# Kernel tuning notes

Measured on AMD Instinct MI355X. Metric: run time of the kernel, lower is better.

The kernel has to match this reference:

```python
import jax, jax.numpy as jnp
import numpy as np
import math

N_TOK = 8192; IN_DIM = 1024; D = 512; HEADS = 8; DH = D // HEADS
M = D // 2; ITERS = 6; SCALE = DH ** -0.5; KRES = 33; NCLS = 2
EPS = 1e-5


def ln(x, g, b):
    mu = jnp.mean(x, -1, keepdims=True)
    var = jnp.var(x, -1, keepdims=True)
    return (x - mu) * jax.lax.rsqrt(var + EPS) * g + b


def moore_penrose_pinv(x):
    # Newton-Schulz iterative pseudo-inverse (lucidrains nystrom-attention)
    col = jnp.abs(x).sum(-1).max()
    row = jnp.abs(x).sum(-2).max()
    z = jnp.swapaxes(x, -1, -2) / (col * row)
    I = jnp.eye(x.shape[-1], dtype=x.dtype)
    for _ in range(ITERS):
        xz = x @ z
        z = 0.25 * z @ (13 * I - xz @ (15 * I - xz @ (7 * I - xz)))
    return z


def nystrom_attn(x, qkv_w, out_w, out_b, conv_w):
    b, n, _ = x.shape
    pad = (-n) % M  # pad at FRONT so seq len divisible by num_landmarks
    xp = jnp.pad(x, ((0, 0), (pad, 0), (0, 0)))
    Np = n + pad
    q, k, v = jnp.split(xp @ qkv_w, 3, axis=-1)
    tohead = lambda t: t.reshape(b, Np, HEADS, DH).transpose(0, 2, 1, 3)  # bhnd
    q = tohead(q) * SCALE; k = tohead(k); v = tohead(v)
    l = Np // M
    q_l = q.reshape(b, HEADS, M, l, DH).mean(3)  # landmark means, bhmd
    k_l = k.reshape(b, HEADS, M, l, DH).mean(3)
    a1 = jax.nn.softmax(jnp.einsum('bhnd,bhmd->bhnm', q, k_l), -1)
    a2 = jax.nn.softmax(jnp.einsum('bhnd,bhmd->bhnm', q_l, k_l), -1)
    a3 = jax.nn.softmax(jnp.einsum('bhmd,bhnd->bhmn', q_l, k), -1)
    out = (a1 @ moore_penrose_pinv(a2)) @ (a3 @ v)
    pc = KRES // 2  # depthwise residual conv over sequence dim (groups=heads)
    out = out + jax.lax.conv_general_dilated(
        v, conv_w, (1, 1), [(pc, pc), (0, 0)],
        dimension_numbers=('NCHW', 'OIHW', 'NCHW'), feature_group_count=HEADS)
    out = out.transpose(0, 2, 1, 3).reshape(b, Np, D)
    return (out @ out_w + out_b)[:, -n:]


def ppeg(x, Hs, Ws, w7, b7, w5, b5, w3, b3):
    b, _, C = x.shape
    cls_tok, feat = x[:, :1], x[:, 1:]
    f = feat.transpose(0, 2, 1).reshape(b, C, Hs, Ws)
    def dw(w, bb, p):
        return jax.lax.conv_general_dilated(
            f, w, (1, 1), [(p, p), (p, p)],
            dimension_numbers=('NCHW', 'OIHW', 'NCHW'),
            feature_group_count=C) + bb[None, :, None, None]
    y = f + dw(w7, b7, 3) + dw(w5, b5, 2) + dw(w3, b3, 1)
    y = y.reshape(b, C, Hs * Ws).transpose(0, 2, 1)
    return jnp.concatenate([cls_tok, y], axis=1)


def setup_inputs() -> dict:
    key = jax.random.key(0)
    ks = jax.random.split(key, 16)
    s = 0.02
    return {
        'x': jax.random.normal(ks[0], (N_TOK, IN_DIM), jnp.float32),
        'fc1_w': jax.random.normal(ks[1], (IN_DIM, D), jnp.float32) * s,
        'fc1_b': jnp.zeros((D,), jnp.float32),
        'cls_token': jax.random.normal(ks[2], (1, 1, D), jnp.float32),
        'ln1_g': jnp.ones((D,), jnp.float32), 'ln1_b': jnp.zeros((D,), jnp.float32),
        'qkv1_w': jax.random.normal(ks[3], (D, 3 * D), jnp.float32) * s,
        'out1_w': jax.random.normal(ks[4], (D, D), jnp.float32) * s,
        'out1_b': jnp.zeros((D,), jnp.float32),
        'conv1_w': jax.random.normal(ks[5], (HEADS, 1, KRES, 1), jnp.float32) * s,
        'ln2_g': jnp.ones((D,), jnp.float32), 'ln2_b': jnp.zeros((D,), jnp.float32),
        'qkv2_w': jax.random.normal(ks[6], (D, 3 * D), jnp.float32) * s,
        'out2_w': jax.random.normal(ks[7], (D, D), jnp.float32) * s,
        'out2_b': jnp.zeros((D,), jnp.float32),
        'conv2_w': jax.random.normal(ks[8], (HEADS, 1, KRES, 1), jnp.float32) * s,
        'pg7_w': jax.random.normal(ks[9], (D, 1, 7, 7), jnp.float32) * s,
        'pg7_b': jnp.zeros((D,), jnp.float32),
        'pg5_w': jax.random.normal(ks[10], (D, 1, 5, 5), jnp.float32) * s,
        'pg5_b': jnp.zeros((D,), jnp.float32),
        'pg3_w': jax.random.normal(ks[11], (D, 1, 3, 3), jnp.float32) * s,
        'pg3_b': jnp.zeros((D,), jnp.float32),
        'norm_g': jnp.ones((D,), jnp.float32), 'norm_b': jnp.zeros((D,), jnp.float32),
        'fc2_w': jax.random.normal(ks[12], (D, NCLS), jnp.float32) * s,
        'fc2_b': jnp.zeros((NCLS,), jnp.float32),
    }


def reference(x, fc1_w, fc1_b, cls_token, ln1_g, ln1_b, qkv1_w, out1_w, out1_b,
              conv1_w, ln2_g, ln2_b, qkv2_w, out2_w, out2_b, conv2_w,
              pg7_w, pg7_b, pg5_w, pg5_b, pg3_w, pg3_b, norm_g, norm_b,
              fc2_w, fc2_b):
    h = jax.nn.relu(x[None].astype(jnp.float32) @ fc1_w + fc1_b)  # [1,N,D]
    n = h.shape[1]
    Hs = Ws = int(math.ceil(math.sqrt(n)))
    add = Hs * Ws - n
    h = jnp.concatenate([h, h[:, :add]], axis=1)  # pad to square by duplication
    h = jnp.concatenate([jnp.broadcast_to(cls_token, (1, 1, D)), h], axis=1)
    h = h + nystrom_attn(ln(h, ln1_g, ln1_b), qkv1_w, out1_w, out1_b, conv1_w)
    h = ppeg(h, Hs, Ws, pg7_w, pg7_b, pg5_w, pg5_b, pg3_w, pg3_b)
    h = h + nystrom_attn(ln(h, ln2_g, ln2_b), qkv2_w, out2_w, out2_b, conv2_w)
    emb = ln(h, norm_g, norm_b)[:, 0]  # cls embedding [1,D]
    logits = emb @ fc2_w + fc2_b
    Y_prob = jax.nn.softmax(logits, -1)
    Y_hat = jnp.argmax(logits, -1)
    return (logits, Y_prob, Y_hat, emb)
```

## Files before the change

### kernel.cpp

```cpp
#include <hip/hip_runtime.h>
#include <math.h>

#define NTOK   8192
#define INDIM  1024
#define NHEAD  8
#define N1     8282
#define NP     8448
#define PAD    166
#define LCH    33
#define SCALE  0.125f
#define HS     91
#define KSPLIT 24
#define KCH    (NP / KSPLIT)

typedef __attribute__((ext_vector_type(8))) _Float16 half8;
typedef __attribute__((ext_vector_type(8))) short short8;
typedef __attribute__((ext_vector_type(4))) float f32x4;
typedef unsigned short ushort_t;

#define GPTR(p) ((const __attribute__((address_space(1))) void*)(p))
#define LPTR(p) ((__attribute__((address_space(3))) void*)(p))

__device__ __forceinline__ ushort_t f2h(float f) {
    union { _Float16 h; ushort_t u; } v; v.h = (_Float16)f;
    return v.u;
}
__device__ __forceinline__ float h2f(ushort_t u) {
    union { ushort_t u; _Float16 h; } v; v.u = u;
    return (float)v.h;
}


__device__ __forceinline__ float blockReduceSumF(float v, float* red, int tid) {
    red[tid] = v; __syncthreads();
    for (int s = 128; s > 0; s >>= 1) {
        if (tid < s) red[tid] += red[tid + s];
        __syncthreads();
    }
    float r = red[0]; __syncthreads();
    return r;
}
__device__ __forceinline__ float blockReduceMaxF(float v, float* red, int tid) {
    red[tid] = v; __syncthreads();
    for (int s = 128; s > 0; s >>= 1) {
        if (tid < s) red[tid] = fmaxf(red[tid], red[tid + s]);
        __syncthreads();
    }
    float r = red[0]; __syncthreads();
    return r;
}

__global__ void zero_k(float* __restrict__ p)
{
    int i = blockIdx.x * 256 + threadIdx.x;
    reinterpret_cast<float4*>(p)[i] = make_float4(0.f, 0.f, 0.f, 0.f);
}

__global__ __launch_bounds__(256) void tcast_k(const float* __restrict__ w, ushort_t* __restrict__ wT,
                                               int K, int N)
{
    __shared__ float tb[32][33];
    int tx = threadIdx.x & 31, ty = threadIdx.x >> 5;
    int n0 = blockIdx.x * 32, k0 = blockIdx.y * 32;
#pragma unroll
    for (int i = 0; i < 4; ++i)
        tb[ty + i * 8][tx] = w[(size_t)(k0 + ty + i * 8) * N + n0 + tx];
    __syncthreads();
#pragma unroll
    for (int i = 0; i < 4; ++i)
        wT[(size_t)(n0 + ty + i * 8) * K + k0 + tx] = f2h(tb[tx][ty + i * 8]);
}

__global__ void bcast_k(const float* __restrict__ x, ushort_t* __restrict__ o)
{
    int i = blockIdx.x * 256 + threadIdx.x;
    float4 v = reinterpret_cast<const float4*>(x)[i];
    ushort4 u;
    u.x = f2h(v.x); u.y = f2h(v.y); u.z = f2h(v.z); u.w = f2h(v.w);
    reinterpret_cast<ushort4*>(o)[i] = u;
}

__global__ __launch_bounds__(256) void gemm_mn_f16(
    const ushort_t* __restrict__ A, const ushort_t* __restrict__ BT,
    const float* __restrict__ bias, const float* __restrict__ res,
    float* __restrict__ C, ushort_t* __restrict__ Ch,
    int Mvalid, int K, int lda, int ldb, int ldc, int relu, int qscale)
{
    __shared__ ushort_t As[128 * 32];
    __shared__ ushort_t Bs[64 * 32];
    const int tid = threadIdx.x;
    const int wave = tid >> 6, lane = tid & 63;
    const int row0 = blockIdx.y * 128, col0 = blockIdx.x * 64;
    const int wr = wave * 32;
    const int aRow = wave * 16 + (lane >> 2);
    const int aChS = (((lane & 3) ^ ((lane >> 3) & 3)) * 8);
    const int bRow = tid >> 2;
    const int bChS = (((tid & 3) ^ ((tid >> 3) & 3)) * 8);
    const int lr = lane & 15, lq = (lane >> 4) * 4;
    const int lks = (((lane >> 4) ^ ((lr >> 1) & 3)) * 8);
    f32x4 acc[2][4] = {};
    for (int k0 = 0; k0 < K; k0 += 32) {
        __syncthreads();
#pragma unroll
        for (int i = 0; i < 2; ++i) {
            const ushort_t* gp = A + (size_t)(row0 + i * 64 + aRow) * lda + k0 + aChS;
            __builtin_amdgcn_global_load_lds(GPTR(gp), LPTR(As + (i * 64 + wave * 16) * 32), 16, 0, 0);
        }
        const ushort_t* gq = BT + (size_t)(col0 + bRow) * ldb + k0 + bChS;
        __builtin_amdgcn_global_load_lds(GPTR(gq), LPTR(Bs + tid * 8), 16, 0, 0);
        __syncthreads();
        half8 af[2], bfr[4];
#pragma unroll
        for (int mi = 0; mi < 2; ++mi)
            af[mi] = *reinterpret_cast<const half8*>(&As[(wr + mi * 16 + lr) * 32 + lks]);
#pragma unroll
        for (int ni = 0; ni < 4; ++ni)
            bfr[ni] = *reinterpret_cast<const half8*>(&Bs[(ni * 16 + lr) * 32 + lks]);
#pragma unroll
        for (int mi = 0; mi < 2; ++mi)
#pragma unroll
            for (int ni = 0; ni < 4; ++ni)
                acc[mi][ni] = __builtin_amdgcn_mfma_f32_16x16x32_f16(af[mi], bfr[ni], acc[mi][ni], 0, 0, 0);
    }
#pragma unroll
    for (int mi = 0; mi < 2; ++mi) {
#pragma unroll
        for (int q = 0; q < 4; ++q) {
            int r = row0 + wr + mi * 16 + lq + q;
            if (r >= Mvalid) continue;
#pragma unroll
            for (int ni = 0; ni < 4; ++ni) {
                int c = col0 + ni * 16 + lr;
                float v = acc[mi][ni][q];
                if (bias) v += bias[c];
                if (res)  v += res[(size_t)r * ldc + c];
                if (relu) v = fmaxf(v, 0.f);
                if (Ch) {
                    if (qscale && c < 512) v *= SCALE;
                    Ch[(size_t)r * ldc + c] = f2h(v);
                } else {
                    C[(size_t)r * ldc + c] = v;
                }
            }
        }
    }
}

__global__ __launch_bounds__(256) void bgemm64_f16(
    const ushort_t* __restrict__ A, const ushort_t* __restrict__ B,
    ushort_t* __restrict__ C, float diag, float ss,
    ushort_t* __restrict__ C2, float diag2, float ss2)
{
    __shared__ ushort_t As[64 * 32];
    __shared__ ushort_t Bs[64 * 32];
    const int h = blockIdx.z;
    const ushort_t* Ah = A + (size_t)h * 65536;
    const ushort_t* Bh = B + (size_t)h * 65536;
    const int tid = threadIdx.x;
    const int wave = tid >> 6, lane = tid & 63;
    const int row0 = blockIdx.y * 64, col0 = blockIdx.x * 64;
    const int wr = (wave >> 1) * 32, wc = (wave & 1) * 32;
    const int aRow = tid >> 2;
    const int aChS = (((tid & 3) ^ ((tid >> 3) & 3)) * 8);
    const int kp = (tid >> 3) & 15, nc = tid & 7;
    const int kk = (kp * 2) ^ ((nc & 3) << 3);
    const int lr = lane & 15, lk = (lane >> 4) * 8, lq = (lane >> 4) * 4;
    const int lks = (((lane >> 4) ^ ((lr >> 1) & 3)) * 8);
    f32x4 acc[2][2] = {};
    for (int k0 = 0; k0 < 256; k0 += 32) {
        __syncthreads();
        const ushort_t* gp = Ah + (size_t)(row0 + aRow) * 256 + k0 + aChS;
        __builtin_amdgcn_global_load_lds(GPTR(gp), LPTR(As + tid * 8), 16, 0, 0);
        if (tid < 128) {
            const ushort_t* bp = Bh + (size_t)(k0 + kp * 2) * 256 + col0 + nc * 8;
            short8 v0 = *reinterpret_cast<const short8*>(bp);
            short8 v1 = *reinterpret_cast<const short8*>(bp + 256);
#pragma unroll
            for (int j = 0; j < 8; ++j) {
                unsigned int pk = ((unsigned int)(ushort_t)v1[j] << 16) | (unsigned int)(ushort_t)v0[j];
                *reinterpret_cast<unsigned int*>(&Bs[(nc * 8 + j) * 32 + kk]) = pk;
            }
        }
        __syncthreads();
        half8 af[2], bfr[2];
#pragma unroll
        for (int mi = 0; mi < 2; ++mi)
            af[mi] = *reinterpret_cast<const half8*>(&As[(wr + mi * 16 + lr) * 32 + lks]);
#pragma unroll
        for (int ni = 0; ni < 2; ++ni) {
            int nn = wc + ni * 16 + lr;
            bfr[ni] = *reinterpret_cast<const half8*>(&Bs[nn * 32 + (lk ^ (((nn >> 3) & 3) << 3))]);
        }
#pragma unroll
        for (int mi = 0; mi < 2; ++mi)
#pragma unroll
            for (int ni = 0; ni < 2; ++ni)
                acc[mi][ni] = __builtin_amdgcn_mfma_f32_16x16x32_f16(af[mi], bfr[ni], acc[mi][ni], 0, 0, 0);
    }
    ushort_t* Chp = C + (size_t)h * 65536;
#pragma unroll
    for (int mi = 0; mi < 2; ++mi)
#pragma unroll
        for (int ni = 0; ni < 2; ++ni)
#pragma unroll
            for (int q = 0; q < 4; ++q) {
                int r = row0 + wr + mi * 16 + lq + q;
                int c = col0 + wc + ni * 16 + lr;
                float v = ss * acc[mi][ni][q];
                if (r == c) v += diag;
                Chp[(size_t)r * 256 + c] = f2h(v);
                if (C2) {
                    float v2 = ss2 * acc[mi][ni][q];
                    if (r == c) v2 += diag2;
                    C2[(size_t)h * 65536 + (size_t)r * 256 + c] = f2h(v2);
                }
            }
}

__global__ __launch_bounds__(256) void hgemm_abT_k(
    const ushort_t* __restrict__ A, long sAh, int lda,
    const ushort_t* __restrict__ BT, long sBh, int ldb,
    ushort_t* __restrict__ C, long sCh, int ldc, int K,
    float* __restrict__ rsum, int sRsum)
{
    __shared__ ushort_t As[128 * 32];
    __shared__ ushort_t Bs[128 * 32];
    const int h = blockIdx.z;
    const ushort_t* Ah = A + (size_t)h * sAh;
    const ushort_t* Bh = BT + (size_t)h * sBh;
    ushort_t* Chp = C + (size_t)h * sCh;
    const int tid = threadIdx.x;
    const int wave = tid >> 6, lane = tid & 63;
    const int row0 = blockIdx.y * 128, col0 = blockIdx.x * 128;
    const int wr = (wave >> 1) * 64, wc = (wave & 1) * 64;
    const int sRow = wave * 16 + (lane >> 2);
    const int sChS = (((lane & 3) ^ ((lane >> 3) & 3)) * 8);
    const int lr = lane & 15, lq = (lane >> 4) * 4;
    const int lks = (((lane >> 4) ^ ((lr >> 1) & 3)) * 8);
    f32x4 acc[4][4] = {};
    for (int k0 = 0; k0 < K; k0 += 32) {
        __syncthreads();
#pragma unroll
        for (int i = 0; i < 2; ++i) {
            const ushort_t* gp = Ah + (size_t)(row0 + i * 64 + sRow) * lda + k0 + sChS;
            __builtin_amdgcn_global_load_lds(GPTR(gp), LPTR(As + (i * 64 + wave * 16) * 32), 16, 0, 0);
            const ushort_t* gq = Bh + (size_t)(col0 + i * 64 + sRow) * ldb + k0 + sChS;
            __builtin_amdgcn_global_load_lds(GPTR(gq), LPTR(Bs + (i * 64 + wave * 16) * 32), 16, 0, 0);
        }
        __syncthreads();
        half8 af[4], bfr[4];
#pragma unroll
        for (int mi = 0; mi < 4; ++mi)
            af[mi] = *reinterpret_cast<const half8*>(&As[(wr + mi * 16 + lr) * 32 + lks]);
#pragma unroll
        for (int ni = 0; ni < 4; ++ni)
            bfr[ni] = *reinterpret_cast<const half8*>(&Bs[(wc + ni * 16 + lr) * 32 + lks]);
#pragma unroll
        for (int mi = 0; mi < 4; ++mi)
#pragma unroll
            for (int ni = 0; ni < 4; ++ni)
                acc[mi][ni] = __builtin_amdgcn_mfma_f32_16x16x32_f16(af[mi], bfr[ni], acc[mi][ni], 0, 0, 0);
    }
#pragma unroll
    for (int mi = 0; mi < 4; ++mi)
#pragma unroll
        for (int q = 0; q < 4; ++q) {
            int r = row0 + wr + mi * 16 + lq + q;
            float s = 0.f;
#pragma unroll
            for (int ni = 0; ni < 4; ++ni) {
                float e = __expf(acc[mi][ni][q]);
                Chp[(size_t)r * ldc + col0 + wc + ni * 16 + lr] = f2h(e);
                s += e;
            }
            for (int off = 8; off; off >>= 1) s += __shfl_xor(s, off, 64);
            if (lr == 0) atomicAdd(&rsum[(size_t)h * sRsum + r], s);
        }
}

__global__ __launch_bounds__(256) void fa1_k(
    const ushort_t* __restrict__ qkv16, const ushort_t* __restrict__ kl,
    const ushort_t* __restrict__ W, ushort_t* __restrict__ attn)
{
    __shared__ ushort_t Pl[128][264];
    __shared__ ushort_t As[128 * 32];
    __shared__ ushort_t Bs[64 * 32];
    __shared__ float rs_l[128];
    const int h = blockIdx.y;
    const int row0 = blockIdx.x * 128;
    const ushort_t* Aq = qkv16 + h * 64;
    const ushort_t* klh = kl + (size_t)h * 16384;
    const ushort_t* Wh = W + (size_t)h * 16384;
    const int tid = threadIdx.x;
    const int wave = tid >> 6, lane = tid & 63;
    const int wr = wave * 32;
    const int aRow = wave * 16 + (lane >> 2);
    const int aChS = (((lane & 3) ^ ((lane >> 3) & 3)) * 8);
    const int bRow = tid >> 2;
    const int bChS = (((tid & 3) ^ ((tid >> 3) & 3)) * 8);
    const int lr = lane & 15, lk = (lane >> 4) * 8, lq = (lane >> 4) * 4;
    const int lks = (((lane >> 4) ^ ((lr >> 1) & 3)) * 8);
    const int kp = (tid >> 3) & 15, ncs = tid & 7;
    const int kk = (kp * 2) ^ ((ncs & 3) << 3);
    float rs[2][4] = {};
    for (int nc0 = 0; nc0 < 256; nc0 += 64) {
        f32x4 acc[2][4] = {};
        for (int k0 = 0; k0 < 64; k0 += 32) {
            __syncthreads();
#pragma unroll
            for (int i = 0; i < 2; ++i) {
                const ushort_t* gp = Aq + (size_t)(row0 + i * 64 + aRow) * 1536 + k0 + aChS;
                __builtin_amdgcn_global_load_lds(GPTR(gp), LPTR(As + (i * 64 + wave * 16) * 32), 16, 0, 0);
            }
            const ushort_t* gq = klh + (size_t)(nc0 + bRow) * 64 + k0 + bChS;
            __builtin_amdgcn_global_load_lds(GPTR(gq), LPTR(Bs + tid * 8), 16, 0, 0);
            __syncthreads();
            half8 af[2], bfr[4];
#pragma unroll
            for (int mi = 0; mi < 2; ++mi)
                af[mi] = *reinterpret_cast<const half8*>(&As[(wr + mi * 16 + lr) * 32 + lks]);
#pragma unroll
            for (int ni = 0; ni < 4; ++ni)
                bfr[ni] = *reinterpret_cast<const half8*>(&Bs[(ni * 16 + lr) * 32 + lks]);
#pragma unroll
            for (int mi = 0; mi < 2; ++mi)
#pragma unroll
                for (int ni = 0; ni < 4; ++ni)
                    acc[mi][ni] = __builtin_amdgcn_mfma_f32_16x16x32_f16(af[mi], bfr[ni], acc[mi][ni], 0, 0, 0);
        }
#pragma unroll
        for (int mi = 0; mi < 2; ++mi)
#pragma unroll
            for (int q = 0; q < 4; ++q) {
                int r = wr + mi * 16 + lq + q;
                float s = 0.f;
#pragma unroll
                for (int ni = 0; ni < 4; ++ni) {
                    float e = __expf(acc[mi][ni][q]);
                    Pl[r][nc0 + ni * 16 + lr] = f2h(e);
                    s += e;
                }
                for (int off = 8; off; off >>= 1) s += __shfl_xor(s, off, 64);
                rs[mi][q] += s;
            }
    }
    if (lr == 0) {
#pragma unroll
        for (int mi = 0; mi < 2; ++mi)
#pragma unroll
            for (int q = 0; q < 4; ++q)
                rs_l[wr + mi * 16 + lq + q] = rs[mi][q];
    }
    __syncthreads();
    f32x4 acc[2][4] = {};
    for (int k0 = 0; k0 < 256; k0 += 32) {
        __syncthreads();
        if (tid < 128) {
            const ushort_t* bp = Wh + (size_t)(k0 + kp * 2) * 64 + ncs * 8;
            short8 v0 = *reinterpret_cast<const short8*>(bp);
            short8 v1 = *reinterpret_cast<const short8*>(bp + 64);
#pragma unroll
            for (int j = 0; j < 8; ++j) {
                unsigned int pk = ((unsigned int)(ushort_t)v1[j] << 16) | (unsigned int)(ushort_t)v0[j];
                *reinterpret_cast<unsigned int*>(&Bs[(ncs * 8 + j) * 32 + kk]) = pk;
            }
        }
        __syncthreads();
        half8 af[2], bfr[4];
#pragma unroll
        for (int mi = 0; mi < 2; ++mi)
            af[mi] = *reinterpret_cast<const half8*>(&Pl[wr + mi * 16 + lr][k0 + lk]);
#pragma unroll
        for (int ni = 0; ni < 4; ++ni) {
            int nn = ni * 16 + lr;
            bfr[ni] = *reinterpret_cast<const half8*>(&Bs[nn * 32 + (lk ^ (((nn >> 3) & 3) << 3))]);
        }
#pragma unroll
        for (int mi = 0; mi < 2; ++mi)
#pragma unroll
            for (int ni = 0; ni < 4; ++ni)
                acc[mi][ni] = __builtin_amdgcn_mfma_f32_16x16x32_f16(af[mi], bfr[ni], acc[mi][ni], 0, 0, 0);
    }
#pragma unroll
    for (int mi = 0; mi < 2; ++mi)
#pragma unroll
        for (int q = 0; q < 4; ++q) {
            int rloc = wr + mi * 16 + lq + q;
            int t = row0 + rloc;
            float inv = 1.f / rs_l[rloc];
#pragma unroll
            for (int ni = 0; ni < 4; ++ni)
                attn[(size_t)t * 512 + h * 64 + ni * 16 + lr] = f2h(acc[mi][ni][q] * inv);
        }
}

__global__ __launch_bounds__(256) void hgemm_pv_k(
    const ushort_t* __restrict__ P, const ushort_t* __restrict__ qkv16,
    float* __restrict__ part)
{
    __shared__ ushort_t As[128 * 32];
    __shared__ ushort_t Bs[64 * 32];
    const int ks = blockIdx.x, row0 = blockIdx.y * 128, h = blockIdx.z;
    const ushort_t* Ph = P + (size_t)h * 256 * NP;
    const ushort_t* V = qkv16 + 1024 + h * 64;
    const int tid = threadIdx.x;
    const int wave = tid >> 6, lane = tid & 63;
    const int wr = wave * 32;
    const int sRow = wave * 16 + (lane >> 2);
    const int sChS = (((lane & 3) ^ ((lane >> 3) & 3)) * 8);
    const int lr = lane & 15, lk = (lane >> 4) * 8, lq = (lane >> 4) * 4;
    const int lks = (((lane >> 4) ^ ((lr >> 1) & 3)) * 8);
    const int kp = (tid >> 3) & 15, nc = tid & 7;
    const int kk = (kp * 2) ^ ((nc & 3) << 3);
    f32x4 acc[2][4] = {};
    for (int k0 = ks * KCH; k0 < (ks + 1) * KCH; k0 += 32) {
        __syncthreads();
#pragma unroll
        for (int i = 0; i < 2; ++i) {
            const ushort_t* gp = Ph + (size_t)(row0 + i * 64 + sRow) * NP + k0 + sChS;
            __builtin_amdgcn_global_load_lds(GPTR(gp), LPTR(As + (i * 64 + wave * 16) * 32), 16, 0, 0);
        }
        if (tid < 128) {
            const ushort_t* bp = V + (size_t)(k0 + kp * 2) * 1536 + nc * 8;
            short8 v0 = *reinterpret_cast<const short8*>(bp);
            short8 v1 = *reinterpret_cast<const short8*>(bp + 1536);
#pragma unroll
            for (int j = 0; j < 8; ++j) {
                unsigned int pk = ((unsigned int)(ushort_t)v1[j] << 16) | (unsigned int)(ushort_t)v0[j];
                *reinterpret_cast<unsigned int*>(&Bs[(nc * 8 + j) * 32 + kk]) = pk;
            }
        }
        __syncthreads();
        half8 af[2], bfr[4];
#pragma unroll
        for (int mi = 0; mi < 2; ++mi)
            af[mi] = *reinterpret_cast<const half8*>(&As[(wr + mi * 16 + lr) * 32 + lks]);
#pragma unroll
        for (int ni = 0; ni < 4; ++ni) {
            int nn = ni * 16 + lr;
            bfr[ni] = *reinterpret_cast<const half8*>(&Bs[nn * 32 + (lk ^ (((nn >> 3) & 3) << 3))]);
        }
#pragma unroll
        for (int mi = 0; mi < 2; ++mi)
#pragma unroll
            for (int ni = 0; ni < 4; ++ni)
                acc[mi][ni] = __builtin_amdgcn_mfma_f32_16x16x32_f16(af[mi], bfr[ni], acc[mi][ni], 0, 0, 0);
    }
    float* pp = part + ((size_t)(ks * 8 + h) * 256) * 64;
#pragma unroll
    for (int mi = 0; mi < 2; ++mi)
#pragma unroll
        for (int q = 0; q < 4; ++q) {
            int r = row0 + wr + mi * 16 + lq + q;
#pragma unroll
            for (int ni = 0; ni < 4; ++ni)
                pp[(size_t)r * 64 + ni * 16 + lr] = acc[mi][ni][q];
        }
}

__global__ __launch_bounds__(256) void pv_reduce_k(const float* __restrict__ part,
                                                   const float* __restrict__ rsum,
                                                   ushort_t* __restrict__ av)
{
    int idx = blockIdx.x * 256 + threadIdx.x;
    int rc = idx >> 6;
    float s = 0.f;
#pragma unroll
    for (int ks = 0; ks < KSPLIT; ++ks)
        s += part[(size_t)ks * 131072 + idx];
    av[idx] = f2h(s / rsum[rc]);
}

__global__ __launch_bounds__(256) void wmat_k(const ushort_t* __restrict__ z,
                                              const ushort_t* __restrict__ av,
                                              ushort_t* __restrict__ W)
{
    int idx = blockIdx.x * 4 + (threadIdx.x >> 6);
    int h = idx >> 8, m = idx & 255, d = threadIdx.x & 63;
    const ushort_t* zp = z + (size_t)h * 65536 + (size_t)m * 256;
    const ushort_t* ap = av + (size_t)h * 16384 + d;
    float acc = 0.f;
    for (int j = 0; j < 256; ++j) acc += h2f(zp[j]) * h2f(ap[(size_t)j * 64]);
    W[((size_t)h * 256 + m) * 64 + d] = f2h(acc);
}

__global__ void fixup_k(const float* __restrict__ cls, float* __restrict__ h)
{
    int i = blockIdx.x * 256 + threadIdx.x;
    if (i < 512) {
        h[i] = cls[i];
    } else {
        int j = i - 512;
        h[(size_t)8193 * 512 + j] = h[512 + j];
    }
}

__global__ __launch_bounds__(256) void ln_pad_k(
    const float* __restrict__ h, const float* __restrict__ g, const float* __restrict__ b,
    ushort_t* __restrict__ out)
{
    int row = blockIdx.x, tid = threadIdx.x;
    __shared__ float red[256];
    ushort_t* o = out + (size_t)row * 512;
    if (row < PAD) { o[tid] = 0; o[tid + 256] = 0; return; }
    const float* x = h + (size_t)(row - PAD) * 512;
    float v0 = x[tid], v1 = x[tid + 256];
    float mu = blockReduceSumF(v0 + v1, red, tid) * (1.f / 512.f);
    float d0 = v0 - mu, d1 = v1 - mu;
    float var = blockReduceSumF(d0 * d0 + d1 * d1, red, tid) * (1.f / 512.f);
    float rstd = rsqrtf(var + 1e-5f);
    o[tid]       = f2h(d0 * rstd * g[tid] + b[tid]);
    o[tid + 256] = f2h(d1 * rstd * g[tid + 256] + b[tid + 256]);
}

__global__ __launch_bounds__(256) void landmark_k(const ushort_t* __restrict__ qkv,
                                                  ushort_t* __restrict__ ql,
                                                  ushort_t* __restrict__ kl)
{
    int idx = blockIdx.x * 4 + (threadIdx.x >> 6);
    int h = idx >> 8, m = idx & 255, d = threadIdx.x & 63;
    const ushort_t* base = qkv + (size_t)(m * LCH) * 1536 + h * 64 + d;
    float sq = 0.f, sk = 0.f;
    for (int i = 0; i < LCH; ++i) {
        sq += h2f(base[(size_t)i * 1536]);
        sk += h2f(base[(size_t)i * 1536 + 512]);
    }
    ql[((size_t)h * 256 + m) * 64 + d] = f2h(sq * (1.f / (float)LCH));
    kl[((size_t)h * 256 + m) * 64 + d] = f2h(sk * (1.f / (float)LCH));
}

__global__ __launch_bounds__(256) void a2_k(
    const ushort_t* __restrict__ ql, const ushort_t* __restrict__ kl, ushort_t* __restrict__ a2)
{
    int h = blockIdx.x >> 8, r = blockIdx.x & 255, tid = threadIdx.x;
    __shared__ float qv[64]; __shared__ float red[256];
    if (tid < 64) qv[tid] = h2f(ql[((size_t)h * 256 + r) * 64 + tid]);
    __syncthreads();
    const ushort_t* kp = kl + ((size_t)h * 256 + tid) * 64;
    float dot = 0.f;
#pragma unroll
    for (int d = 0; d < 64; ++d) dot += qv[d] * h2f(kp[d]);
    float mx = blockReduceMaxF(dot, red, tid);
    float e = expf(dot - mx);
    float s = blockReduceSumF(e, red, tid);
    a2[((size_t)h * 256 + r) * 256 + tid] = f2h(e / s);
}

__global__ __launch_bounds__(256) void colsum_k(const ushort_t* __restrict__ a2, float* __restrict__ cs)
{
    int h = blockIdx.x >> 8, c = blockIdx.x & 255;
    __shared__ float red[256];
    float v = fabsf(h2f(a2[(size_t)h * 65536 + (size_t)threadIdx.x * 256 + c]));
    float s = blockReduceSumF(v, red, threadIdx.x);
    if (!threadIdx.x) cs[blockIdx.x] = s;
}
__global__ __launch_bounds__(256) void pinv_scal_k(const float* __restrict__ cs, float* __restrict__ scal)
{
    int tid = threadIdx.x; __shared__ float red[256];
    float m2 = -1e30f;
    for (int i = tid; i < 2048; i += 256) m2 = fmaxf(m2, cs[i]);
    m2 = blockReduceMaxF(m2, red, tid);
    if (!tid) scal[0] = 1.f / m2;
}
__global__ __launch_bounds__(256) void zinit_k(const ushort_t* __restrict__ a2, const float* __restrict__ scal,
                                               ushort_t* __restrict__ z)
{
    int h = blockIdx.x >> 8, r = blockIdx.x & 255, c = threadIdx.x;
    z[(size_t)h * 65536 + (size_t)r * 256 + c] =
        f2h(h2f(a2[(size_t)h * 65536 + (size_t)c * 256 + r]) * scal[0]);
}

#define CTT 64
__global__ __launch_bounds__(256) void conv2_k(const ushort_t* __restrict__ qkv,
                                               const float* __restrict__ cw,
                                               ushort_t* __restrict__ attn)
{
    __shared__ float vt[CTT + 32][64];
    int t0 = blockIdx.x * CTT;
    int h = blockIdx.y;
    int tid = threadIdx.x;
    for (int s = tid; s < (CTT + 32) * 8; s += 256) {
        int row = s >> 3, q8 = s & 7;
        int tt = t0 - 16 + row;
        if (tt >= 0 && tt < NP) {
            short8 v = *reinterpret_cast<const short8*>(qkv + (size_t)tt * 1536 + 1024 + h * 64 + q8 * 8);
#pragma unroll
            for (int j = 0; j < 8; ++j) vt[row][q8 * 8 + j] = h2f((ushort_t)v[j]);
        } else {
#pragma unroll
            for (int j = 0; j < 8; ++j) vt[row][q8 * 8 + j] = 0.f;
        }
    }
    float w33[33];
#pragma unroll
    for (int j = 0; j < 33; ++j) w33[j] = cw[h * 33 + j];
    __syncthreads();
    int c = tid & 63, tr = tid >> 6;
    float win[48];
#pragma unroll
    for (int j = 0; j < 48; ++j) win[j] = vt[tr * 16 + j][c];
#pragma unroll
    for (int i = 0; i < 16; ++i) {
        float acc = 0.f;
#pragma unroll
        for (int j = 0; j < 33; ++j) acc += w33[j] * win[i + j];
        size_t idx = (size_t)(t0 + tr * 16 + i) * 512 + h * 64 + c;
        attn[idx] = f2h(h2f(attn[idx]) + acc);
    }
}

#define PTS  16
#define PIT  22
#define PITT (PIT*PIT)
#define PCG  8
#define PSTR 12
__global__ __launch_bounds__(256) void ppeg_tiled_k(
    const float* __restrict__ hin,
    const float* __restrict__ w7, const float* __restrict__ b7,
    const float* __restrict__ w5, const float* __restrict__ b5,
    const float* __restrict__ w3, const float* __restrict__ b3,
    float* __restrict__ hout)
{
    __shared__ float inb[PITT][PSTR];
    __shared__ float wcT[49][PCG];
    __shared__ float bs[PCG];
    int tid = threadIdx.x;
    int c0 = blockIdx.z * PCG;
    int ty0 = blockIdx.y * PTS, tx0 = blockIdx.x * PTS;
    if (blockIdx.x == 0 && blockIdx.y == 0 && tid < PCG)
        hout[c0 + tid] = hin[c0 + tid];
    for (int idx = tid; idx < PITT * 2; idx += 256) {
        int tok = idx >> 1, q = idx & 1;
        int gy = ty0 - 3 + tok / PIT, gx = tx0 - 3 + tok % PIT;
        float4 v = make_float4(0.f, 0.f, 0.f, 0.f);
        if (gy >= 0 && gy < HS && gx >= 0 && gx < HS)
            v = *reinterpret_cast<const float4*>(hin + (size_t)(1 + gy * HS + gx) * 512 + c0 + q * 4);
        *reinterpret_cast<float4*>(&inb[tok][q * 4]) = v;
    }
    for (int idx = tid; idx < PCG * 49; idx += 256) {
        int c = idx / 49, t = idx % 49;
        int ky = t / 7, kx = t % 7, dy = ky - 3, dx = kx - 3;
        float w = w7[(size_t)(c0 + c) * 49 + t];
        if (dy >= -2 && dy <= 2 && dx >= -2 && dx <= 2)
            w += w5[(size_t)(c0 + c) * 25 + (dy + 2) * 5 + (dx + 2)];
        if (dy >= -1 && dy <= 1 && dx >= -1 && dx <= 1)
            w += w3[(size_t)(c0 + c) * 9 + (dy + 1) * 3 + (dx + 1)];
        wcT[t][c] = w;
    }
    if (tid < PCG) bs[tid] = b7[c0 + tid] + b5[c0 + tid] + b3[c0 + tid];
    __syncthreads();
    int oy = tid >> 4, ox = tid & 15;
    int gy = ty0 + oy, gx = tx0 + ox;
    if (gy >= HS || gx >= HS) return;
    float acc[PCG];
    {
        const float* cp = &inb[(oy + 3) * PIT + ox + 3][0];
        float4 i0 = *reinterpret_cast<const float4*>(cp);
        float4 i1 = *reinterpret_cast<const float4*>(cp + 4);
        acc[0] = i0.x + bs[0]; acc[1] = i0.y + bs[1]; acc[2] = i0.z + bs[2]; acc[3] = i0.w + bs[3];
        acc[4] = i1.x + bs[4]; acc[5] = i1.y + bs[5]; acc[6] = i1.z + bs[6]; acc[7] = i1.w + bs[7];
    }
#pragma unroll
    for (int ky = 0; ky < 7; ++ky)
#pragma unroll
        for (int kx = 0; kx < 7; ++kx) {
            int t = ky * 7 + kx;
            const float* dp = &inb[(oy + ky) * PIT + ox + kx][0];
            float4 d0 = *reinterpret_cast<const float4*>(dp);
            float4 d1 = *reinterpret_cast<const float4*>(dp + 4);
            float4 w0 = *reinterpret_cast<const float4*>(&wcT[t][0]);
            float4 w1 = *reinterpret_cast<const float4*>(&wcT[t][4]);
            acc[0] += w0.x * d0.x; acc[1] += w0.y * d0.y;
            acc[2] += w0.z * d0.z; acc[3] += w0.w * d0.w;
            acc[4] += w1.x * d1.x; acc[5] += w1.y * d1.y;
            acc[6] += w1.z * d1.z; acc[7] += w1.w * d1.w;
        }
    float* out = hout + (size_t)(1 + gy * HS + gx) * 512 + c0;
    *reinterpret_cast<float4*>(out)     = make_float4(acc[0], acc[1], acc[2], acc[3]);
    *reinterpret_cast<float4*>(out + 4) = make_float4(acc[4], acc[5], acc[6], acc[7]);
}

__global__ __launch_bounds__(256) void final_k(const float* __restrict__ h,
                                               const float* __restrict__ g, const float* __restrict__ bb,
                                               const float* __restrict__ w, const float* __restrict__ fb,
                                               float* __restrict__ out)
{
    __shared__ float red[256];
    int tid = threadIdx.x;
    float v0 = h[tid], v1 = h[tid + 256];
    float mu = blockReduceSumF(v0 + v1, red, tid) * (1.f / 512.f);
    float d0 = v0 - mu, d1 = v1 - mu;
    float var = blockReduceSumF(d0 * d0 + d1 * d1, red, tid) * (1.f / 512.f);
    float rstd = rsqrtf(var + 1e-5f);
    float e0 = d0 * rstd * g[tid] + bb[tid];
    float e1 = d1 * rstd * g[tid + 256] + bb[tid + 256];
    out[5 + tid] = e0;
    out[5 + 256 + tid] = e1;
    float l0p = e0 * w[tid * 2] + e1 * w[(tid + 256) * 2];
    float l1p = e0 * w[tid * 2 + 1] + e1 * w[(tid + 256) * 2 + 1];
    float l0 = blockReduceSumF(l0p, red, tid);
    float l1 = blockReduceSumF(l1p, red, tid);
    if (!tid) {
        l0 += fb[0]; l1 += fb[1];
        out[0] = l0; out[1] = l1;
        float mx = fmaxf(l0, l1);
        float p0 = expf(l0 - mx), p1 = expf(l1 - mx);
        float si = 1.f / (p0 + p1);
        out[2] = p0 * si; out[3] = p1 * si;
        out[4] = (l1 > l0) ? 1.f : 0.f;
    }
}

struct WsPtrs {
    float *h, *h2, *cs, *scal, *rsum3, *part;
    ushort_t *xbB, *qkv16, *ql16, *kl16, *a2h, *zh, *z2h, *xzh, *t1h, *t2h;
    ushort_t *av16, *W16, *qkvT, *outT, *x16, *fc1T, *S16;
};

static void run_attn(float* hbuf, const float* ln_g, const float* ln_b,
                     const float* qkv_w, const float* out_w, const float* out_b,
                     const float* conv_w, const WsPtrs& P, hipStream_t s)
{
    tcast_k<<<dim3(1536 / 32, 512 / 32), 256, 0, s>>>(qkv_w, P.qkvT, 512, 1536);
    tcast_k<<<dim3(512 / 32, 512 / 32), 256, 0, s>>>(out_w, P.outT, 512, 512);
    ln_pad_k<<<NP, 256, 0, s>>>(hbuf, ln_g, ln_b, P.xbB);
    gemm_mn_f16<<<dim3(1536 / 64, NP / 128), 256, 0, s>>>(P.xbB, P.qkvT, nullptr, nullptr,
                                                          nullptr, P.qkv16, NP, 512, 512, 512, 1536, 0, 1);
    landmark_k<<<512, 256, 0, s>>>(P.qkv16, P.ql16, P.kl16);
    a2_k<<<2048, 256, 0, s>>>(P.ql16, P.kl16, P.a2h);
    colsum_k<<<2048, 256, 0, s>>>(P.a2h, P.cs);
    pinv_scal_k<<<1, 256, 0, s>>>(P.cs, P.scal);
    zinit_k<<<2048, 256, 0, s>>>(P.a2h, P.scal, P.zh);
    ushort_t* za = P.zh; ushort_t* zb = P.z2h;
    for (int it = 0; it < 6; ++it) {
        bgemm64_f16<<<dim3(4, 4, 8), 256, 0, s>>>(P.a2h, za, P.xzh, 0.f, 1.f, P.t1h, 7.f, -1.f);
        bgemm64_f16<<<dim3(4, 4, 8), 256, 0, s>>>(P.xzh, P.t1h, P.t2h, 15.f, -1.f, nullptr, 0.f, 0.f);
        bgemm64_f16<<<dim3(4, 4, 8), 256, 0, s>>>(P.xzh, P.t2h, P.t1h, 13.f, -1.f, nullptr, 0.f, 0.f);
        bgemm64_f16<<<dim3(4, 4, 8), 256, 0, s>>>(za, P.t1h, zb, 0.f, 0.25f, nullptr, 0.f, 0.f);
        ushort_t* tmp = za; za = zb; zb = tmp;
    }
    zero_k<<<2, 256, 0, s>>>(P.rsum3);
    hgemm_abT_k<<<dim3(NP / 128, 2, 8), 256, 0, s>>>(P.ql16, 16384, 64,
                                                     P.qkv16 + 512, 64, 1536,
                                                     P.S16, (long)256 * NP, NP, 64,
                                                     P.rsum3, 256);
    hgemm_pv_k<<<dim3(KSPLIT, 2, 8), 256, 0, s>>>(P.S16, P.qkv16, P.part);
    pv_reduce_k<<<512, 256, 0, s>>>(P.part, P.rsum3, P.av16);
    wmat_k<<<512, 256, 0, s>>>(za, P.av16, P.W16);
    fa1_k<<<dim3(NP / 128, 8), 256, 0, s>>>(P.qkv16, P.kl16, P.W16, P.xbB);
    conv2_k<<<dim3(NP / CTT, 8), 256, 0, s>>>(P.qkv16, conv_w, P.xbB);
    gemm_mn_f16<<<dim3(512 / 64, (N1 + 127) / 128), 256, 0, s>>>(P.xbB + (size_t)PAD * 512, P.outT,
                                                                 out_b, hbuf, hbuf, nullptr,
                                                                 N1, 512, 512, 512, 512, 0, 0);
}

extern "C" void kernel_launch(void* const* d_in, const int* in_sizes, int n_in,
                              void* d_out, int out_size, void* d_ws, size_t ws_size,
                              hipStream_t stream)
{
    (void)in_sizes; (void)n_in; (void)out_size; (void)ws_size;
    const float* x       = (const float*)d_in[0];
    const float* fc1_w   = (const float*)d_in[1];
    const float* fc1_b   = (const float*)d_in[2];
    const float* cls_tok = (const float*)d_in[3];
    const float* ln1_g   = (const float*)d_in[4];
    const float* ln1_b   = (const float*)d_in[5];
    const float* qkv1_w  = (const float*)d_in[6];
    const float* out1_w  = (const float*)d_in[7];
    const float* out1_b  = (const float*)d_in[8];
    const float* conv1_w = (const float*)d_in[9];
    const float* ln2_g   = (const float*)d_in[10];
    const float* ln2_b   = (const float*)d_in[11];
    const float* qkv2_w  = (const float*)d_in[12];
    const float* out2_w  = (const float*)d_in[13];
    const float* out2_b  = (const float*)d_in[14];
    const float* conv2_w = (const float*)d_in[15];
    const float* pg7_w   = (const float*)d_in[16];
    const float* pg7_b   = (const float*)d_in[17];
    const float* pg5_w   = (const float*)d_in[18];
    const float* pg5_b   = (const float*)d_in[19];
    const float* pg3_w   = (const float*)d_in[20];
    const float* pg3_b   = (const float*)d_in[21];
    const float* norm_g  = (const float*)d_in[22];
    const float* norm_b  = (const float*)d_in[23];
    const float* fc2_w   = (const float*)d_in[24];
    const float* fc2_b   = (const float*)d_in[25];

    float* ws = (float*)d_ws;
    WsPtrs P;
    float* cur = ws;
    P.h     = cur; cur += (size_t)N1 * 512;
    P.h2    = cur; cur += (size_t)N1 * 512;
    P.xbB   = (ushort_t*)cur; cur += (size_t)NP * 512 / 2;
    P.qkv16 = (ushort_t*)cur; cur += (size_t)NP * 1536 / 2;
    P.ql16  = (ushort_t*)cur; cur += 65536;
    P.kl16  = (ushort_t*)cur; cur += 65536;
    P.a2h   = (ushort_t*)cur; cur += 262144;
    P.zh    = (ushort_t*)cur; cur += 262144;
    P.z2h   = (ushort_t*)cur; cur += 262144;
    P.xzh   = (ushort_t*)cur; cur += 262144;
    P.t1h   = (ushort_t*)cur; cur += 262144;
    P.t2h   = (ushort_t*)cur; cur += 262144;
    P.av16  = (ushort_t*)cur; cur += 65536;
    P.W16   = (ushort_t*)cur; cur += 65536;
    P.cs    = cur; cur += 2048;
    P.scal  = cur; cur += 64;
    P.qkvT  = (ushort_t*)cur; cur += 393216 + 64;
    P.outT  = (ushort_t*)cur; cur += 131072 + 64;
    P.rsum3 = cur; cur += 2048;
    P.part  = cur; cur += (size_t)KSPLIT * 131072;
    P.S16   = (ushort_t*)cur; cur += (size_t)8 * 256 * NP / 2;
    P.x16   = P.S16;
    P.fc1T  = P.S16 + (size_t)NTOK * INDIM;

    bcast_k<<<(NTOK * INDIM) / 1024, 256, 0, stream>>>(x, P.x16);
    tcast_k<<<dim3(512 / 32, 1024 / 32), 256, 0, stream>>>(fc1_w, P.fc1T, 1024, 512);
    gemm_mn_f16<<<dim3(512 / 64, NTOK / 128), 256, 0, stream>>>(P.x16, P.fc1T, fc1_b, nullptr,
                                                                P.h + 512, nullptr,
                                                                NTOK, 1024, 1024, 1024, 512, 1, 0);
    fixup_k<<<180, 256, 0, stream>>>(cls_tok, P.h);
    run_attn(P.h, ln1_g, ln1_b, qkv1_w, out1_w, out1_b, conv1_w, P, stream);
    ppeg_tiled_k<<<dim3(6, 6, 512 / PCG), 256, 0, stream>>>(P.h, pg7_w, pg7_b, pg5_w, pg5_b,
                                                            pg3_w, pg3_b, P.h2);
    run_attn(P.h2, ln2_g, ln2_b, qkv2_w, out2_w, out2_b, conv2_w, P, stream);
    final_k<<<1, 256, 0, stream>>>(P.h2, norm_g, norm_b, fc2_w, fc2_b, (float*)d_out);
}
```

Baseline: 782.4 us.

## Fuse landmark-query scores, exp and PV product into one split-K flash kernel

Replaces the separate kernel that computed exp(q_l·k^T) into a large fp16 score buffer, followed by a split-K P·V GEMM, with one kernel. Each block streams 64-token chunks of K, computes the exponentiated scores into LDS, accumulates row sums in registers and immediately multiplies by V. This avoids writing and re-reading the 8×256×8448 score matrix through global memory. In exchange the work is split 33 ways along the tokens, so partial sums grow, and each chunk now carries extra barriers.

```diff
diff --git a/kernel.cpp b/kernel.cpp
--- a/kernel.cpp
+++ b/kernel.cpp
@@ -10,8 +10,8 @@
 #define LCH    33
 #define SCALE  0.125f
 #define HS     91
-#define KSPLIT 24
-#define KCH    (NP / KSPLIT)
+#define KS3    33
+#define KC3    (NP / KS3)
 
 typedef __attribute__((ext_vector_type(8))) _Float16 half8;
 typedef __attribute__((ext_vector_type(8))) short short8;
@@ -217,65 +217,128 @@
             }
 }
 
-__global__ __launch_bounds__(256) void hgemm_abT_k(
-    const ushort_t* __restrict__ A, long sAh, int lda,
-    const ushort_t* __restrict__ BT, long sBh, int ldb,
-    ushort_t* __restrict__ C, long sCh, int ldc, int K,
-    float* __restrict__ rsum, int sRsum)
-{
-    __shared__ ushort_t As[128 * 32];
-    __shared__ ushort_t Bs[128 * 32];
-    const int h = blockIdx.z;
-    const ushort_t* Ah = A + (size_t)h * sAh;
-    const ushort_t* Bh = BT + (size_t)h * sBh;
-    ushort_t* Chp = C + (size_t)h * sCh;
+__global__ __launch_bounds__(256) void fs3_k(
+    const ushort_t* __restrict__ ql, const ushort_t* __restrict__ qkv16,
+    float* __restrict__ part, float* __restrict__ rsum)
+{
+    __shared__ ushort_t Qs[2][128 * 32];
+    __shared__ ushort_t Bs[64 * 32];
+    __shared__ ushort_t Pl[128][72];
+    const int ks = blockIdx.x, row0 = blockIdx.y * 128, h = blockIdx.z;
+    const ushort_t* Ah = ql + (size_t)h * 16384;
+    const ushort_t* Kh = qkv16 + 512 + h * 64;
+    const ushort_t* Vh = qkv16 + 1024 + h * 64;
     const int tid = threadIdx.x;
     const int wave = tid >> 6, lane = tid & 63;
-    const int row0 = blockIdx.y * 128, col0 = blockIdx.x * 128;
-    const int wr = (wave >> 1) * 64, wc = (wave & 1) * 64;
-    const int sRow = wave * 16 + (lane >> 2);
-    const int sChS = (((lane & 3) ^ ((lane >> 3) & 3)) * 8);
-    const int lr = lane & 15, lq = (lane >> 4) * 4;
+    const int wr = wave * 32;
+    const int aRow = wave * 16 + (lane >> 2);
+    const int aChS = (((lane & 3) ^ ((lane >> 3) & 3)) * 8);
+    const int bRow = tid >> 2;
+    const int bChS = (((tid & 3) ^ ((tid >> 3) & 3)) * 8);
+    const int lr = lane & 15, lk = (lane >> 4) * 8, lq = (lane >> 4) * 4;
     const int lks = (((lane >> 4) ^ ((lr >> 1) & 3)) * 8);
-    f32x4 acc[4][4] = {};
-    for (int k0 = 0; k0 < K; k0 += 32) {
-        __syncthreads();
+    const int kp = (tid >> 3) & 15, nc = tid & 7;
+    const int kk = (kp * 2) ^ ((nc & 3) << 3);
+#pragma unroll
+    for (int hh = 0; hh < 2; ++hh)
 #pragma unroll
         for (int i = 0; i < 2; ++i) {
-            const ushort_t* gp = Ah + (size_t)(row0 + i * 64 + sRow) * lda + k0 + sChS;
-            __builtin_amdgcn_global_load_lds(GPTR(gp), LPTR(As + (i * 64 + wave * 16) * 32), 16, 0, 0);
-            const ushort_t* gq = Bh + (size_t)(col0 + i * 64 + sRow) * ldb + k0 + sChS;
-            __builtin_amdgcn_global_load_lds(GPTR(gq), LPTR(Bs + (i * 64 + wave * 16) * 32), 16, 0, 0);
-        }
-        __syncthreads();
-        half8 af[4], bfr[4];
-#pragma unroll
-        for (int mi = 0; mi < 4; ++mi)
-            af[mi] = *reinterpret_cast<const half8*>(&As[(wr + mi * 16 + lr) * 32 + lks]);
-#pragma unroll
-        for (int ni = 0; ni < 4; ++ni)
-            bfr[ni] = *reinterpret_cast<const half8*>(&Bs[(wc + ni * 16 + lr) * 32 + lks]);
-#pragma unroll
-        for (int mi = 0; mi < 4; ++mi)
+            const ushort_t* gp = Ah + (size_t)(row0 + i * 64 + aRow) * 64 + hh * 32 + aChS;
+            __builtin_amdgcn_global_load_lds(GPTR(gp), LPTR(Qs[hh] + (i * 64 + wave * 16) * 32), 16, 0, 0);
+        }
+    f32x4 aco[2][4] = {};
+    float rs[2][4] = {};
+    for (int c = 0; c < KC3; c += 64) {
+        const int tok0 = ks * KC3 + c;
+        f32x4 acs[2][4] = {};
+#pragma unroll
+        for (int k0 = 0; k0 < 64; k0 += 32) {
+            __syncthreads();
+            const ushort_t* gq = Kh + (size_t)(tok0 + bRow) * 1536 + k0 + bChS;
+            __builtin_amdgcn_global_load_lds(GPTR(gq), LPTR(Bs + tid * 8), 16, 0, 0);
+            __syncthreads();
+            half8 af[2], bfr[4];
+#pragma unroll
+            for (int mi = 0; mi < 2; ++mi)
+                af[mi] = *reinterpret_cast<const half8*>(&Qs[k0 >> 5][(wr + mi * 16 + lr) * 32 + lks]);
 #pragma unroll
             for (int ni = 0; ni < 4; ++ni)
-                acc[mi][ni] = __builtin_amdgcn_mfma_f32_16x16x32_f16(af[mi], bfr[ni], acc[mi][ni], 0, 0, 0);
-    }
-#pragma unroll
-    for (int mi = 0; mi < 4; ++mi)
+                bfr[ni] = *reinterpret_cast<const half8*>(&Bs[(ni * 16 + lr) * 32 + lks]);
+#pragma unroll
+            for (int mi = 0; mi < 2; ++mi)
+#pragma unroll
+                for (int ni = 0; ni < 4; ++ni)
+                    acs[mi][ni] = __builtin_amdgcn_mfma_f32_16x16x32_f16(af[mi], bfr[ni], acs[mi][ni], 0, 0, 0);
+        }
+#pragma unroll
+        for (int mi = 0; mi < 2; ++mi)
+#pragma unroll
+            for (int q = 0; q < 4; ++q) {
+                int r = wr + mi * 16 + lq + q;
+                float s = 0.f;
+#pragma unroll
+                for (int ni = 0; ni < 4; ++ni) {
+                    float e = __expf(acs[mi][ni][q]);
+                    Pl[r][ni * 16 + lr] = f2h(e);
+                    s += e;
+                }
+                for (int off = 8; off; off >>= 1) s += __shfl_xor(s, off, 64);
+                rs[mi][q] += s;
+            }
+#pragma unroll
+        for (int k0 = 0; k0 < 64; k0 += 32) {
+            __syncthreads();
+            if (tid < 128) {
+                const ushort_t* bp = Vh + (size_t)(tok0 + k0 + kp * 2) * 1536 + nc * 8;
+                short8 v0 = *reinterpret_cast<const short8*>(bp);
+                short8 v1 = *reinterpret_cast<const short8*>(bp + 1536);
+#pragma unroll
+                for (int j = 0; j < 8; ++j) {
+                    unsigned int pk = ((unsigned int)(ushort_t)v1[j] << 16) | (unsigned int)(ushort_t)v0[j];
+                    *reinterpret_cast<unsigned int*>(&Bs[(nc * 8 + j) * 32 + kk]) = pk;
+                }
+            }
+            __syncthreads();
+            half8 af[2], bfr[4];
+#pragma unroll
+            for (int mi = 0; mi < 2; ++mi)
+                af[mi] = *reinterpret_cast<const half8*>(&Pl[wr + mi * 16 + lr][k0 + lk]);
+#pragma unroll
+            for (int ni = 0; ni < 4; ++ni) {
+                int nn = ni * 16 + lr;
+                bfr[ni] = *reinterpret_cast<const half8*>(&Bs[nn * 32 + (lk ^ (((nn >> 3) & 3) << 3))]);
+            }
+#pragma unroll
+            for (int mi = 0; mi < 2; ++mi)
+#pragma unroll
+                for (int ni = 0; ni < 4; ++ni)
+                    aco[mi][ni] = __builtin_amdgcn_mfma_f32_16x16x32_f16(af[mi], bfr[ni], aco[mi][ni], 0, 0, 0);
+        }
+    }
+    float* pp = part + (size_t)(ks * 8 + h) * 16384;
+#pragma unroll
+    for (int mi = 0; mi < 2; ++mi)
 #pragma unroll
         for (int q = 0; q < 4; ++q) {
             int r = row0 + wr + mi * 16 + lq + q;
-            float s = 0.f;
-#pragma unroll
-            for (int ni = 0; ni < 4; ++ni) {
-                float e = __expf(acc[mi][ni][q]);
-                Chp[(size_t)r * ldc + col0 + wc + ni * 16 + lr] = f2h(e);
-                s += e;
-            }
-            for (int off = 8; off; off >>= 1) s += __shfl_xor(s, off, 64);
-            if (lr == 0) atomicAdd(&rsum[(size_t)h * sRsum + r], s);
-        }
+#pragma unroll
+            for (int ni = 0; ni < 4; ++ni)
+                pp[(size_t)r * 64 + ni * 16 + lr] = aco[mi][ni][q];
+            if (lr == 0) atomicAdd(&rsum[h * 256 + r], rs[mi][q]);
+        }
+}
+
+__global__ __launch_bounds__(256) void pv_reduce_k(const float* __restrict__ part,
+                                                   const float* __restrict__ rsum,
+                                                   ushort_t* __restrict__ av)
+{
+    int idx = blockIdx.x * 256 + threadIdx.x;
+    int rc = idx >> 6;
+    float s = 0.f;
+#pragma unroll
+    for (int ks = 0; ks < KS3; ++ks)
+        s += part[(size_t)ks * 131072 + idx];
+    av[idx] = f2h(s / rsum[rc]);
 }
 
 __global__ __launch_bounds__(256) void fa1_k(
@@ -394,83 +457,6 @@
         }
 }
 
-__global__ __launch_bounds__(256) void hgemm_pv_k(
-    const ushort_t* __restrict__ P, const ushort_t* __restrict__ qkv16,
-    float* __restrict__ part)
-{
-    __shared__ ushort_t As[128 * 32];
-    __shared__ ushort_t Bs[64 * 32];
-    const int ks = blockIdx.x, row0 = blockIdx.y * 128, h = blockIdx.z;
-    const ushort_t* Ph = P + (size_t)h * 256 * NP;
-    const ushort_t* V = qkv16 + 1024 + h * 64;
-    const int tid = threadIdx.x;
-    const int wave = tid >> 6, lane = tid & 63;
-    const int wr = wave * 32;
-    const int sRow = wave * 16 + (lane >> 2);
-    const int sChS = (((lane & 3) ^ ((lane >> 3) & 3)) * 8);
-    const int lr = lane & 15, lk = (lane >> 4) * 8, lq = (lane >> 4) * 4;
-    const int lks = (((lane >> 4) ^ ((lr >> 1) & 3)) * 8);
-    const int kp = (tid >> 3) & 15, nc = tid & 7;
-    const int kk = (kp * 2) ^ ((nc & 3) << 3);
-    f32x4 acc[2][4] = {};
-    for (int k0 = ks * KCH; k0 < (ks + 1) * KCH; k0 += 32) {
-        __syncthreads();
-#pragma unroll
-        for (int i = 0; i < 2; ++i) {
-            const ushort_t* gp = Ph + (size_t)(row0 + i * 64 + sRow) * NP + k0 + sChS;
-            __builtin_amdgcn_global_load_lds(GPTR(gp), LPTR(As + (i * 64 + wave * 16) * 32), 16, 0, 0);
-        }
-        if (tid < 128) {
-            const ushort_t* bp = V + (size_t)(k0 + kp * 2) * 1536 + nc * 8;
-            short8 v0 = *reinterpret_cast<const short8*>(bp);
-            short8 v1 = *reinterpret_cast<const short8*>(bp + 1536);
-#pragma unroll
-            for (int j = 0; j < 8; ++j) {
-                unsigned int pk = ((unsigned int)(ushort_t)v1[j] << 16) | (unsigned int)(ushort_t)v0[j];
-                *reinterpret_cast<unsigned int*>(&Bs[(nc * 8 + j) * 32 + kk]) = pk;
-            }
-        }
-        __syncthreads();
-        half8 af[2], bfr[4];
-#pragma unroll
-        for (int mi = 0; mi < 2; ++mi)
-            af[mi] = *reinterpret_cast<const half8*>(&As[(wr + mi * 16 + lr) * 32 + lks]);
-#pragma unroll
-        for (int ni = 0; ni < 4; ++ni) {
-            int nn = ni * 16 + lr;
-            bfr[ni] = *reinterpret_cast<const half8*>(&Bs[nn * 32 + (lk ^ (((nn >> 3) & 3) << 3))]);
-        }
-#pragma unroll
-        for (int mi = 0; mi < 2; ++mi)
-#pragma unroll
-            for (int ni = 0; ni < 4; ++ni)
-                acc[mi][ni] = __builtin_amdgcn_mfma_f32_16x16x32_f16(af[mi], bfr[ni], acc[mi][ni], 0, 0, 0);
-    }
-    float* pp = part + ((size_t)(ks * 8 + h) * 256) * 64;
-#pragma unroll
-    for (int mi = 0; mi < 2; ++mi)
-#pragma unroll
-        for (int q = 0; q < 4; ++q) {
-            int r = row0 + wr + mi * 16 + lq + q;
-#pragma unroll
-            for (int ni = 0; ni < 4; ++ni)
-                pp[(size_t)r * 64 + ni * 16 + lr] = acc[mi][ni][q];
-        }
-}
-
-__global__ __launch_bounds__(256) void pv_reduce_k(const float* __restrict__ part,
-                                                   const float* __restrict__ rsum,
-                                                   ushort_t* __restrict__ av)
-{
-    int idx = blockIdx.x * 256 + threadIdx.x;
-    int rc = idx >> 6;
-    float s = 0.f;
-#pragma unroll
-    for (int ks = 0; ks < KSPLIT; ++ks)
-        s += part[(size_t)ks * 131072 + idx];
-    av[idx] = f2h(s / rsum[rc]);
-}
-
 __global__ __launch_bounds__(256) void wmat_k(const ushort_t* __restrict__ z,
                                               const ushort_t* __restrict__ av,
                                               ushort_t* __restrict__ W)
@@ -740,11 +726,7 @@
         ushort_t* tmp = za; za = zb; zb = tmp;
     }
     zero_k<<<2, 256, 0, s>>>(P.rsum3);
-    hgemm_abT_k<<<dim3(NP / 128, 2, 8), 256, 0, s>>>(P.ql16, 16384, 64,
-                                                     P.qkv16 + 512, 64, 1536,
-                                                     P.S16, (long)256 * NP, NP, 64,
-                                                     P.rsum3, 256);
-    hgemm_pv_k<<<dim3(KSPLIT, 2, 8), 256, 0, s>>>(P.S16, P.qkv16, P.part);
+    fs3_k<<<dim3(KS3, 2, 8), 256, 0, s>>>(P.ql16, P.qkv16, P.part, P.rsum3);
     pv_reduce_k<<<512, 256, 0, s>>>(P.part, P.rsum3, P.av16);
     wmat_k<<<512, 256, 0, s>>>(za, P.av16, P.W16);
     fa1_k<<<dim3(NP / 128, 8), 256, 0, s>>>(P.qkv16, P.kl16, P.W16, P.xbB);
@@ -808,7 +790,7 @@
     P.qkvT  = (ushort_t*)cur; cur += 393216 + 64;
     P.outT  = (ushort_t*)cur; cur += 131072 + 64;
     P.rsum3 = cur; cur += 2048;
-    P.part  = cur; cur += (size_t)KSPLIT * 131072;
+    P.part  = cur; cur += (size_t)KS3 * 131072;
     P.S16   = (ushort_t*)cur; cur += (size_t)8 * 256 * NP / 2;
     P.x16   = P.S16;
     P.fc1T  = P.S16 + (size_t)NTOK * INDIM;
```

Result: faster. 736.6 us, median of 2 (-5.9%).
